# Optimization experiments

Measured on AMD Instinct MI355X. Metric: run time of the kernel, lower is better.

## Reference

```python
import jax, jax.numpy as jnp
import numpy as np

K = 16  # nsample for knn_point

def _bn(x, g, b):
    # inference-mode BatchNorm1d folded to per-channel affine (running stats 0/1)
    return x * g[None, :, None] + b[None, :, None]

def _knn(xyz, k):
    # xyz: [B,3,N] -> idx [B,N,k] of k nearest neighbors (squared L2)
    p = xyz.transpose(0, 2, 1)                                   # [B,N,3]
    sq = jnp.sum(p * p, axis=-1)                                 # [B,N]
    d = sq[:, :, None] + sq[:, None, :] - 2.0 * jnp.einsum('bnc,bmc->bnm', p, p)
    _, idx = jax.lax.top_k(-d, k)
    return idx

def _gather(hT, idx):
    # hT: [B,N,C], idx: [B,N,K] -> [B,N,K,C]
    return jax.vmap(lambda a, i: a[i])(hT, idx)

def setup_inputs():
    key = jax.random.key(0)
    ks = jax.random.split(key, 12)
    B, N, C = 16, 2048, 128
    def w(k, shape, fan):
        return jax.random.normal(k, shape, jnp.float32) * (1.0 / np.sqrt(fan))
    o = jnp.ones; z = jnp.zeros
    return {
        'points': jax.random.normal(ks[0], (B, 6, N), jnp.float32),
        'label': jax.random.uniform(ks[1], (B, 1, 16), jnp.float32),
        'We1': w(ks[2], (C, 6), 6), 'ge1': o(C), 'be1': z(C),
        'We2': w(ks[3], (C, C), C), 'ge2': o(C), 'be2': z(C),
        'W1': w(ks[4], (3, C, C), C), 'g1': o((3, C)), 'b1': z((3, C)),
        'W2': w(ks[5], (3, C, C), C), 'g2': o((3, C)), 'b2': z((3, C)),
        'Wf': w(ks[6], (1024, 3 * C), 3 * C), 'gf': o(1024), 'bf': z(1024),
        'Wl': w(ks[7], (64, 16), 16), 'gl': o(64), 'bl': z(64),
        'Wc1': w(ks[8], (512, 3136), 3136), 'bc1': z(512), 'gc1': o(512), 'bb1': z(512),
        'Wc2': w(ks[9], (256, 512), 512), 'bc2': z(256), 'gc2': o(256), 'bb2': z(256),
        'Wc3': w(ks[10], (50, 256), 256), 'bc3': z(50),
    }

def reference(points, label, We1, ge1, be1, We2, ge2, be2, W1, g1, b1, W2, g2, b2,
              Wf, gf, bf, Wl, gl, bl, Wc1, bc1, gc1, bb1, Wc2, bc2, gc2, bb2, Wc3, bc3):
    B, _, N = points.shape
    x = points[:, :6, :]
    xyz = x[:, :3, :]
    idx = _knn(xyz, K)                                            # [B,N,16]
    # input embedding: two conv1x1 + BN + ReLU
    h = jax.nn.relu(_bn(jnp.einsum('oc,bcn->bon', We1, x), ge1, be1))
    h = jax.nn.relu(_bn(jnp.einsum('oc,bcn->bon', We2, h), ge2, be2))
    xs = []
    for i in range(3):  # PVDSA_Res blocks (simplified: conv-BN-ReLU, kNN max-agg, conv-BN + residual)
        t = jax.nn.relu(_bn(jnp.einsum('oc,bcn->bon', W1[i], h), g1[i], b1[i]))
        nbr = _gather(t.transpose(0, 2, 1), idx)                  # [B,N,K,C]
        m = nbr.max(axis=2).transpose(0, 2, 1)                    # [B,C,N]
        h = jax.nn.relu(_bn(jnp.einsum('oc,bcn->bon', W2[i], m), g2[i], b2[i]) + h)
        xs.append(h)
    xcat = jnp.concatenate(xs, axis=1)                            # [B,384,N]
    xf = jax.nn.leaky_relu(_bn(jnp.einsum('oc,bcn->bon', Wf, xcat), gf, bf), 0.2)  # [B,1024,N]
    x_max = xf.max(axis=-1)                                       # [B,1024]
    x_avg = xf.mean(axis=-1)                                      # [B,1024]
    cls = jnp.broadcast_to(label.transpose(0, 2, 1), (B, 16, N))
    lab = jax.nn.leaky_relu(_bn(jnp.einsum('oc,bcn->bon', Wl, cls), gl, bl), 0.2)  # [B,64,N]
    glob = jnp.concatenate([
        jnp.broadcast_to(x_max[:, :, None], (B, 1024, N)),
        jnp.broadcast_to(x_avg[:, :, None], (B, 1024, N)),
        lab], axis=1)
    xa = jnp.concatenate([xf, glob], axis=1)                      # [B,3136,N]
    c = jax.nn.relu(_bn(jnp.einsum('oc,bcn->bon', Wc1, xa) + bc1[None, :, None], gc1, bb1))
    c = jax.nn.relu(_bn(jnp.einsum('oc,bcn->bon', Wc2, c) + bc2[None, :, None], gc2, bb2))
    out = jnp.einsum('oc,bcn->bon', Wc3, c) + bc3[None, :, None]  # [B,50,N]
    return out
```

## Files before the change

### kernel.cpp

```cpp
#include <hip/hip_runtime.h>
#include <cstdint>
#include <cstddef>

#define DEVINL __device__ __forceinline__

typedef float    f32x4 __attribute__((ext_vector_type(4)));
typedef _Float16 f16x8 __attribute__((ext_vector_type(8)));
typedef _Float16 f16x4 __attribute__((ext_vector_type(4)));

constexpr int BB = 16, NN = 2048, MM = 32768;

constexpr size_t OFF_WE1 = 0;
constexpr size_t OFF_WE2 = OFF_WE1 + 128 * 64 * 2;
constexpr size_t OFF_W1  = OFF_WE2 + 128 * 128 * 2;
constexpr size_t OFF_W2  = OFF_W1  + 3 * 128 * 128 * 2;
constexpr size_t OFF_WF  = OFF_W2  + 3 * 128 * 128 * 2;
constexpr size_t OFF_WC1 = OFF_WF  + 1024 * 384 * 2;
constexpr size_t OFF_WC2 = OFF_WC1 + 512 * 1024 * 2;
constexpr size_t OFF_WC3 = OFF_WC2 + 256 * 512 * 2;
constexpr size_t OFF_BC2 = OFF_WC3 + 128 * 256 * 2;
constexpr size_t OFF_BC3 = OFF_BC2 + 256 * 4;
constexpr size_t OFF_CVEC= OFF_BC3 + 128 * 4;
constexpr size_t OFF_PMAX= OFF_CVEC+ 16 * 512 * 4;
constexpr size_t OFF_PSUM= OFF_PMAX+ 16 * 16 * 1024 * 4;
constexpr size_t OFF_IDX = OFF_PSUM+ 16 * 16 * 1024 * 4;
constexpr size_t OFF_R1  = 8ull << 20;
constexpr size_t OFF_X0  = OFF_R1;
constexpr size_t OFF_HT  = OFF_R1 + (4ull  << 20);
constexpr size_t OFF_TT  = OFF_R1 + (12ull << 20);
constexpr size_t OFF_MT  = OFF_R1 + (20ull << 20);
constexpr size_t OFF_C1  = OFF_R1;
constexpr size_t OFF_XCAT= OFF_R1 + (32ull << 20);
constexpr size_t OFF_C2  = OFF_XCAT;
constexpr size_t OFF_XF  = OFF_XCAT + (24ull << 20);

__global__ __launch_bounds__(256) void fold_all_kernel(
    const float* We1, const float* ge1, const float* We2, const float* ge2,
    const float* W1,  const float* g1,  const float* W2,  const float* g2,
    const float* Wf,  const float* gf,  const float* Wc1, const float* gc1,
    const float* Wc2, const float* gc2, const float* Wc3,
    const float* gc2b, const float* bc2, const float* bb2, const float* bc3,
    const float* pts, char* ws)
{
    const int bid = blockIdx.x;
    const int tid = threadIdx.x;

    if (bid == 4704) {
        ((float*)(ws + OFF_BC2))[tid] = gc2b[tid] * bc2[tid] + bb2[tid];
        return;
    }
    if (bid == 4705) {
        if (tid < 128) ((float*)(ws + OFF_BC3))[tid] = (tid < 50) ? bc3[tid] : 0.f;
        return;
    }
    if (bid >= 4706) {
        int m = (bid - 4706) * 256 + tid;
        int b = m >> 11, n = m & 2047;
        const float* ps = pts + (size_t)b * 6 * 2048 + n;
        _Float16 tmp[64];
#pragma unroll
        for (int c = 0; c < 64; ++c) tmp[c] = (_Float16)0.f;
#pragma unroll
        for (int c = 0; c < 6; ++c) tmp[c] = (_Float16)ps[(size_t)c << 11];
        _Float16* dst = (_Float16*)(ws + OFF_X0) + (size_t)m * 64;
#pragma unroll
        for (int v = 0; v < 8; ++v) *(f16x8*)(dst + v * 8) = *(const f16x8*)(tmp + v * 8);
        return;
    }

    int id, base;
    if      (bid < 32)   { id = 0;  base = 0;    }
    else if (bid < 96)   { id = 1;  base = 32;   }
    else if (bid < 160)  { id = 2;  base = 96;   }
    else if (bid < 224)  { id = 3;  base = 160;  }
    else if (bid < 288)  { id = 4;  base = 224;  }
    else if (bid < 352)  { id = 5;  base = 288;  }
    else if (bid < 416)  { id = 6;  base = 352;  }
    else if (bid < 480)  { id = 7;  base = 416;  }
    else if (bid < 2016) { id = 8;  base = 480;  }
    else if (bid < 4064) { id = 9;  base = 2016; }
    else if (bid < 4576) { id = 10; base = 4064; }
    else                 { id = 11; base = 4576; }

    const float* src = nullptr; const float* g = nullptr; _Float16* dst = nullptr;
    int O = 0, K = 0, lds = 0, Kp = 0;
    switch (id) {
        case 0:  src = We1; g = ge1; O = 128; K = 6;    lds = 6;    Kp = 64;   dst = (_Float16*)(ws + OFF_WE1); break;
        case 1:  src = We2; g = ge2; O = 128; K = 128;  lds = 128;  Kp = 128;  dst = (_Float16*)(ws + OFF_WE2); break;
        case 2: case 3: case 4: {
            int i = id - 2;
            src = W1 + (size_t)i * 16384; g = g1 + i * 128; O = 128; K = 128; lds = 128; Kp = 128;
            dst = (_Float16*)(ws + OFF_W1) + (size_t)i * 16384; break; }
        case 5: case 6: case 7: {
            int i = id - 5;
            src = W2 + (size_t)i * 16384; g = g2 + i * 128; O = 128; K = 128; lds = 128; Kp = 128;
            dst = (_Float16*)(ws + OFF_W2) + (size_t)i * 16384; break; }
        case 8:  src = Wf;  g = gf;  O = 1024; K = 384;  lds = 384;  Kp = 384;  dst = (_Float16*)(ws + OFF_WF);  break;
        case 9:  src = Wc1; g = gc1; O = 512;  K = 1024; lds = 3136; Kp = 1024; dst = (_Float16*)(ws + OFF_WC1); break;
        case 10: src = Wc2; g = gc2; O = 256;  K = 512;  lds = 512;  Kp = 512;  dst = (_Float16*)(ws + OFF_WC2); break;
        default: src = Wc3; g = nullptr; O = 50; K = 256; lds = 256; Kp = 256;  dst = (_Float16*)(ws + OFF_WC3); break;
    }
    int e = (bid - base) * 256 + tid;
    int o = e / Kp, k = e - o * Kp;
    float v = 0.f;
    if (o < O && k < K) {
        v = src[(size_t)o * lds + k];
        if (g) v *= g[o];
    }
    dst[e] = (_Float16)v;
}

DEVINL float knn_dist(const float4 pq, const float4 pm) {
    float t = pq.x * pm.x;
    t = fmaf(pq.y, pm.y, t);
    t = fmaf(pq.z, pm.z, t);
    return fmaf(-2.f, t, pm.w);
}

#define KNN_DINS(X) do { \
    const float x_ = (X); \
    d15 = __builtin_amdgcn_fmed3f(x_, d14, d15); \
    d14 = __builtin_amdgcn_fmed3f(x_, d13, d14); \
    d13 = __builtin_amdgcn_fmed3f(x_, d12, d13); \
    d12 = __builtin_amdgcn_fmed3f(x_, d11, d12); \
    d11 = __builtin_amdgcn_fmed3f(x_, d10, d11); \
    d10 = __builtin_amdgcn_fmed3f(x_, d9,  d10); \
    d9  = __builtin_amdgcn_fmed3f(x_, d8,  d9);  \
    d8  = __builtin_amdgcn_fmed3f(x_, d7,  d8);  \
    d7  = __builtin_amdgcn_fmed3f(x_, d6,  d7);  \
    d6  = __builtin_amdgcn_fmed3f(x_, d5,  d6);  \
    d5  = __builtin_amdgcn_fmed3f(x_, d4,  d5);  \
    d4  = __builtin_amdgcn_fmed3f(x_, d3,  d4);  \
    d3  = __builtin_amdgcn_fmed3f(x_, d2,  d3);  \
    d2  = __builtin_amdgcn_fmed3f(x_, d1,  d2);  \
    d1  = __builtin_amdgcn_fmed3f(x_, d0,  d1);  \
    d0  = __builtin_amdgcn_fmed3f(x_, -3.4e38f, d0); \
} while (0)

#define KNN_CE(A, B) { const float lo_ = fminf(A, B), hi_ = fmaxf(A, B); A = lo_; B = hi_; }

#define KNN_MERGE(OFF) do { \
    const float n0  = __shfl_xor(d0,  OFF), n1  = __shfl_xor(d1,  OFF), \
                n2  = __shfl_xor(d2,  OFF), n3  = __shfl_xor(d3,  OFF), \
                n4  = __shfl_xor(d4,  OFF), n5  = __shfl_xor(d5,  OFF), \
                n6  = __shfl_xor(d6,  OFF), n7  = __shfl_xor(d7,  OFF), \
                n8  = __shfl_xor(d8,  OFF), n9  = __shfl_xor(d9,  OFF), \
                n10 = __shfl_xor(d10, OFF), n11 = __shfl_xor(d11, OFF), \
                n12 = __shfl_xor(d12, OFF), n13 = __shfl_xor(d13, OFF), \
                n14 = __shfl_xor(d14, OFF), n15 = __shfl_xor(d15, OFF); \
    d0  = fminf(d0,  n15); d1  = fminf(d1,  n14); d2  = fminf(d2,  n13); d3  = fminf(d3,  n12); \
    d4  = fminf(d4,  n11); d5  = fminf(d5,  n10); d6  = fminf(d6,  n9);  d7  = fminf(d7,  n8);  \
    d8  = fminf(d8,  n7);  d9  = fminf(d9,  n6);  d10 = fminf(d10, n5);  d11 = fminf(d11, n4);  \
    d12 = fminf(d12, n3);  d13 = fminf(d13, n2);  d14 = fminf(d14, n1);  d15 = fminf(d15, n0);  \
    KNN_CE(d0, d8)  KNN_CE(d1, d9)  KNN_CE(d2, d10) KNN_CE(d3, d11) \
    KNN_CE(d4, d12) KNN_CE(d5, d13) KNN_CE(d6, d14) KNN_CE(d7, d15) \
    KNN_CE(d0, d4)  KNN_CE(d1, d5)  KNN_CE(d2, d6)  KNN_CE(d3, d7)  \
    KNN_CE(d8, d12) KNN_CE(d9, d13) KNN_CE(d10,d14) KNN_CE(d11,d15) \
    KNN_CE(d0, d2)  KNN_CE(d1, d3)  KNN_CE(d4, d6)  KNN_CE(d5, d7)  \
    KNN_CE(d8, d10) KNN_CE(d9, d11) KNN_CE(d12,d14) KNN_CE(d13,d15) \
    KNN_CE(d0, d1)  KNN_CE(d2, d3)  KNN_CE(d4, d5)  KNN_CE(d6, d7)  \
    KNN_CE(d8, d9)  KNN_CE(d10,d11) KNN_CE(d12,d13) KNN_CE(d14,d15) \
} while (0)

__global__ __launch_bounds__(256) void knn_kernel(const float* __restrict__ pts, int* __restrict__ idxout)
{
    __shared__ float4 P[2048];
    __shared__ unsigned short buf[32][96];
    __shared__ int cnt[32];
    __shared__ int wcnt[32];
    const int tid = threadIdx.x;
    const int b = blockIdx.x;
    const float* pb = pts + (size_t)b * 6 * 2048;
    for (int i = tid; i < 2048; i += 256) {
        float x = pb[i];
        float y = pb[2048 + i];
        float z = pb[4096 + i];
        P[i] = make_float4(x, y, z, x * x + y * y + z * z);
    }
    if (tid < 32) { cnt[tid] = 0; wcnt[tid] = 0; }
    __syncthreads();

    const int p = tid & 7;
    const int g = tid >> 3;
    const int q = blockIdx.y * 32 + g;
    const float4 pq = P[q];

    float d0 = 3.4e38f, d1 = 3.4e38f, d2 = 3.4e38f, d3 = 3.4e38f;
#pragma unroll 4
    for (int it = 0; it < 256; ++it) {
        const float4 pm = P[it * 8 + p];
        const float x = knn_dist(pq, pm);
        d3 = __builtin_amdgcn_fmed3f(x, d2, d3);
        d2 = __builtin_amdgcn_fmed3f(x, d1, d2);
        d1 = __builtin_amdgcn_fmed3f(x, d0, d1);
        d0 = fminf(x, d0);
    }
    float d4 = 3.4e38f, d5 = 3.4e38f, d6 = 3.4e38f, d7 = 3.4e38f,
          d8 = 3.4e38f, d9 = 3.4e38f, d10 = 3.4e38f, d11 = 3.4e38f,
          d12 = 3.4e38f, d13 = 3.4e38f, d14 = 3.4e38f, d15 = 3.4e38f;
    KNN_MERGE(1);
    KNN_MERGE(2);
    KNN_MERGE(4);
    const float tub = d15;

#pragma unroll 4
    for (int it = 0; it < 256; ++it) {
        const int m = it * 8 + p;
        const float d = knn_dist(pq, P[m]);
        if (d <= tub) {
            const int pos = atomicAdd(&cnt[g], 1);
            if (pos < 96) buf[g][pos] = (unsigned short)m;
        }
    }
    int C = cnt[g];
    if (C > 96) C = 96;

    d0 = 3.4e38f; d1 = 3.4e38f; d2 = 3.4e38f; d3 = 3.4e38f;
    d4 = 3.4e38f; d5 = 3.4e38f; d6 = 3.4e38f; d7 = 3.4e38f;
    d8 = 3.4e38f; d9 = 3.4e38f; d10 = 3.4e38f; d11 = 3.4e38f;
    d12 = 3.4e38f; d13 = 3.4e38f; d14 = 3.4e38f; d15 = 3.4e38f;
    for (int j = p; j < C; j += 8) {
        const int m = buf[g][j];
        const float x = knn_dist(pq, P[m]);
        KNN_DINS(x);
    }
    KNN_MERGE(1);
    KNN_MERGE(2);
    KNN_MERGE(4);
    const float t = d15;

    int* op = idxout + (((size_t)(b << 11) + q) << 4);
    for (int j = p; j < C; j += 8) {
        const int m = buf[g][j];
        const float d = knn_dist(pq, P[m]);
        if (d <= t) {
            const int pos = atomicAdd(&wcnt[g], 1);
            if (pos < 16) op[pos] = m;
        }
    }
}

__global__ __launch_bounds__(512, 2) void gemm256(
    const _Float16* __restrict__ W, const _Float16* __restrict__ X,
    _Float16* __restrict__ Y, const float* __restrict__ bias,
    int Kp, int ldX, int ldY, int Opad, int act, int biasPerBatch,
    float* __restrict__ pmax, float* __restrict__ psum)
{
    __shared__ _Float16 SH[65536];
    const int tid  = threadIdx.x;
    const int lane = tid & 63, wave = tid >> 6;
    const int r = lane & 15, quad = lane >> 4;
    const int wo = wave & 3, wm = wave >> 2;
    const int m_blk = blockIdx.x * 256, o_blk = blockIdx.y * 256;
    const int nt = Kp >> 6;

    f32x4 acc[4][8];
#pragma unroll
    for (int a = 0; a < 4; ++a)
#pragma unroll
        for (int c = 0; c < 8; ++c) acc[a][c] = (f32x4){0.f, 0.f, 0.f, 0.f};

    auto STAGE_HALF = [&](int mat, int tile, int h) {
        const int d = tile & 1;
        _Float16* base = SH + (size_t)(((d * 2 + mat) * 2 + h) << 13);
#pragma unroll
        for (int i = 0; i < 2; ++i) {
            const int g  = ((wave * 2 + i) << 6) + lane;
            const int R  = g >> 2, s2 = g & 3;
            const int K4 = s2 ^ ((R >> 1) & 3);
            const int gk = (tile << 6) + (h << 5) + (K4 << 3);
            const _Float16* src = (mat == 0)
                ? W + (size_t)(o_blk + R) * Kp + gk
                : X + (size_t)(m_blk + R) * ldX + gk;
            __builtin_amdgcn_global_load_lds(
                (const __attribute__((address_space(1))) unsigned int*)src,
                (__attribute__((address_space(3))) unsigned int*)(base + ((wave * 2 + i) << 9)),
                16, 0, 0);
        }
    };

    STAGE_HALF(0, 0, 0); STAGE_HALF(1, 0, 0);
    STAGE_HALF(0, 0, 1); STAGE_HALF(1, 0, 1);
    if (nt > 1) { STAGE_HALF(0, 1, 0); STAGE_HALF(1, 1, 0); }

    f16x8 af[4];
    for (int t = 0; t < nt; ++t) {
        const int d = t & 1;
#pragma unroll
        for (int ph = 0; ph < 4; ++ph) {
            const int ks = ph >> 1, mh = ph & 1;
            if (ph == 0) {
                if (t == nt - 1) asm volatile("s_waitcnt vmcnt(4)" ::: "memory");
                else             asm volatile("s_waitcnt vmcnt(8)" ::: "memory");
            } else if (ph == 2) {
                if (t == nt - 1) asm volatile("s_waitcnt vmcnt(0)" ::: "memory");
                else             asm volatile("s_waitcnt vmcnt(8)" ::: "memory");
            }
            __builtin_amdgcn_sched_barrier(0);
            __builtin_amdgcn_s_barrier();
            __builtin_amdgcn_sched_barrier(0);

            if (mh == 0) {
#pragma unroll
                for (int oi = 0; oi < 4; ++oi) {
                    const int R  = (wo << 6) + (oi << 4) + r;
                    const int s2 = quad ^ ((R >> 1) & 3);
                    af[oi] = *(const f16x8*)(SH + (size_t)(((d * 2 + 0) * 2 + ks) << 13)
                                                + (size_t)(((R << 2) + s2) << 3));
                }
            }
            f16x8 bf[4];
#pragma unroll
            for (int j = 0; j < 4; ++j) {
                const int mi = (mh << 2) + j;
                const int R  = (wm << 7) + (mi << 4) + r;
                const int s2 = quad ^ ((R >> 1) & 3);
                bf[j] = *(const f16x8*)(SH + (size_t)(((d * 2 + 1) * 2 + ks) << 13)
                                            + (size_t)(((R << 2) + s2) << 3));
            }

            if (ph == 0)      { if (t + 1 < nt) STAGE_HALF(0, t + 1, 1); }
            else if (ph == 1) { if (t + 1 < nt) STAGE_HALF(1, t + 1, 1); }
            else if (ph == 2) { if (t + 2 < nt) STAGE_HALF(0, t + 2, 0); }
            else              { if (t + 2 < nt) STAGE_HALF(1, t + 2, 0); }

            __builtin_amdgcn_s_setprio(1);
#pragma unroll
            for (int oi = 0; oi < 4; ++oi)
#pragma unroll
                for (int j = 0; j < 4; ++j)
                    acc[oi][(mh << 2) + j] =
                        __builtin_amdgcn_mfma_f32_16x16x32_f16(af[oi], bf[j], acc[oi][(mh << 2) + j], 0, 0, 0);
            __builtin_amdgcn_s_setprio(0);
            __builtin_amdgcn_sched_barrier(0);
        }
    }
    __syncthreads();

    const int bb = biasPerBatch ? (m_blk >> 11) * Opad : 0;
    _Float16* OT = SH;
#pragma unroll
    for (int oi = 0; oi < 4; ++oi) {
        const int ol = (wo << 6) + (oi << 4) + (quad << 2);
        const f32x4 bv = *(const f32x4*)(bias + bb + o_blk + ol);
#pragma unroll
        for (int mi = 0; mi < 8; ++mi) {
            const int row = (wm << 7) + (mi << 4) + r;
            f32x4 v = acc[oi][mi] + bv;
            f16x4 ov;
#pragma unroll
            for (int j = 0; j < 4; ++j) {
                float x = v[j];
                if (act == 1)      x = (x > 0.f) ? x : 0.0f;
                else if (act == 2) x = (x > 0.f) ? x : 0.2f * x;
                ov[j] = (_Float16)x;
            }
            const int s = (ol >> 2) ^ (row & 31);
            *(f16x4*)(OT + row * 256 + s * 4) = ov;
        }
    }
    __syncthreads();
#pragma unroll
    for (int p2 = 0; p2 < 16; ++p2) {
        const int g = (p2 << 9) + tid;
        const int row = g >> 5, c = g & 31;
        const int s0 = ((c << 1)) ^ (row & 31);
        const int s1 = ((c << 1) | 1) ^ (row & 31);
        f16x4 a  = *(const f16x4*)(OT + row * 256 + s0 * 4);
        f16x4 b2 = *(const f16x4*)(OT + row * 256 + s1 * 4);
        f16x8 o8;
        o8[0] = a[0]; o8[1] = a[1]; o8[2] = a[2]; o8[3] = a[3];
        o8[4] = b2[0]; o8[5] = b2[1]; o8[6] = b2[2]; o8[7] = b2[3];
        *(f16x8*)(Y + (size_t)(m_blk + row) * ldY + o_blk + (c << 3)) = o8;
    }

    if (pmax) {
        const int cg = tid & 63, h8 = tid >> 6;
        float mx0 = -3.4e38f, mx1 = -3.4e38f, mx2 = -3.4e38f, mx3 = -3.4e38f;
        float sm0 = 0.f, sm1 = 0.f, sm2 = 0.f, sm3 = 0.f;
#pragma unroll
        for (int rr = 0; rr < 32; ++rr) {
            const int row = (h8 << 5) + rr;
            const f16x4 v = *(const f16x4*)(OT + row * 256 + ((cg ^ (row & 31)) << 2));
            const float x0 = (float)v[0], x1 = (float)v[1], x2 = (float)v[2], x3 = (float)v[3];
            mx0 = fmaxf(mx0, x0); sm0 += x0;
            mx1 = fmaxf(mx1, x1); sm1 += x1;
            mx2 = fmaxf(mx2, x2); sm2 += x2;
            mx3 = fmaxf(mx3, x3); sm3 += x3;
        }
        __syncthreads();
        float* PR = (float*)SH;
        float* pw = PR + (size_t)(((h8 << 8) + (cg << 2)) << 1);
        pw[0] = mx0; pw[1] = sm0; pw[2] = mx1; pw[3] = sm1;
        pw[4] = mx2; pw[5] = sm2; pw[6] = mx3; pw[7] = sm3;
        __syncthreads();
        if (tid < 256) {
            float M = -3.4e38f, S = 0.f;
#pragma unroll
            for (int h2 = 0; h2 < 8; ++h2) {
                M = fmaxf(M, PR[(size_t)(((h2 << 8) + tid) << 1)]);
                S += PR[(size_t)(((h2 << 8) + tid) << 1) + 1];
            }
            const int b2 = m_blk >> 11, mt = (m_blk >> 8) & 7;
            pmax[((size_t)((b2 << 3) + mt) << 10) + o_blk + tid] = M;
            psum[((size_t)((b2 << 3) + mt) << 10) + o_blk + tid] = S;
        }
    }
}

template<int TM>
__global__ __launch_bounds__(256) void gemm_tile(
    const _Float16* __restrict__ W, const _Float16* __restrict__ X,
    _Float16* __restrict__ Y, float* __restrict__ Y32,
    const float* __restrict__ bias, const _Float16* __restrict__ Res,
    int Kp, int ldX, int xoff, int ldY, int yoff, int Opad,
    int act, int biasPerBatch, int ldR, int roff, int Olimit)
{
    constexpr int MI = TM / 32;
    constexpr int ASZ = 128 * 64;
    constexpr int BSZ = TM * 64;
    __shared__ _Float16 SH[2 * (ASZ + BSZ)];

    const int tid  = threadIdx.x;
    const int lane = tid & 63, wave = tid >> 6;
    const int r = lane & 15, quad = lane >> 4;
    const int m_blk = blockIdx.x * TM, o_blk = blockIdx.y * 128;
    const int oh = (wave >> 1) * 64, mh = (wave & 1) * (TM / 2);

    f32x4 acc[4][MI];
#pragma unroll
    for (int a = 0; a < 4; ++a)
#pragma unroll
        for (int c = 0; c < MI; ++c) acc[a][c] = (f32x4){0.f, 0.f, 0.f, 0.f};

    const int srow  = wave * 8 + (lane >> 3);
    const int sslot = lane & 7;

    auto STAGE = [&](int bufi, int k0) {
        _Float16* As = SH + bufi * (ASZ + BSZ);
        _Float16* Bs = As + ASZ;
#pragma unroll
        for (int t = 0; t < 4; ++t) {
            const int rowA = t * 32 + srow;
            const int gk = k0 + ((sslot ^ (rowA & 7)) << 3);
            const _Float16* gA = W + (size_t)(o_blk + rowA) * Kp + gk;
            __builtin_amdgcn_global_load_lds(
                (const __attribute__((address_space(1))) unsigned int*)gA,
                (__attribute__((address_space(3))) unsigned int*)(As + t * 2048 + wave * 512),
                16, 0, 0);
        }
#pragma unroll
        for (int t = 0; t < TM / 32; ++t) {
            const int rowB = t * 32 + srow;
            const int gk = k0 + ((sslot ^ (rowB & 7)) << 3);
            const _Float16* gB = X + (size_t)(m_blk + rowB) * ldX + xoff + gk;
            __builtin_amdgcn_global_load_lds(
                (const __attribute__((address_space(1))) unsigned int*)gB,
                (__attribute__((address_space(3))) unsigned int*)(Bs + t * 2048 + wave * 512),
                16, 0, 0);
        }
    };

    const int nt = Kp >> 6;
    STAGE(0, 0);
    int cur = 0;
    for (int t = 0; t < nt; ++t) {
        if (t + 1 < nt) {
            STAGE(cur ^ 1, (t + 1) << 6);
            if constexpr (TM == 128) asm volatile("s_waitcnt vmcnt(8)" ::: "memory");
            else                     asm volatile("s_waitcnt vmcnt(6)" ::: "memory");
        } else {
            asm volatile("s_waitcnt vmcnt(0)" ::: "memory");
        }
        __builtin_amdgcn_sched_barrier(0);
        __builtin_amdgcn_s_barrier();
        asm volatile("" ::: "memory");

        const _Float16* As = SH + cur * (ASZ + BSZ);
        const _Float16* Bs = As + ASZ;
        __builtin_amdgcn_s_setprio(1);
#pragma unroll
        for (int ks = 0; ks < 2; ++ks) {
            f16x8 af[4], bf[MI];
#pragma unroll
            for (int oi = 0; oi < 4; ++oi) {
                const int row = oh + oi * 16 + r;
                const int slot = (ks * 4 + quad) ^ (row & 7);
                af[oi] = *(const f16x8*)(As + row * 64 + slot * 8);
            }
#pragma unroll
            for (int mi = 0; mi < MI; ++mi) {
                const int row = mh + mi * 16 + r;
                const int slot = (ks * 4 + quad) ^ (row & 7);
                bf[mi] = *(const f16x8*)(Bs + row * 64 + slot * 8);
            }
#pragma unroll
            for (int oi = 0; oi < 4; ++oi)
#pragma unroll
                for (int mi = 0; mi < MI; ++mi)
                    acc[oi][mi] = __builtin_amdgcn_mfma_f32_16x16x32_f16(af[oi], bf[mi], acc[oi][mi], 0, 0, 0);
        }
        __builtin_amdgcn_s_setprio(0);
        asm volatile("" ::: "memory");
        __builtin_amdgcn_s_barrier();
        cur ^= 1;
    }

    const int bb = biasPerBatch ? (m_blk >> 11) * Opad : 0;
    __syncthreads();

    if (Y32) {
#pragma unroll
        for (int oi = 0; oi < 4; ++oi) {
            const int og = o_blk + oh + oi * 16 + quad * 4;
            const f32x4 bv = *(const f32x4*)(bias + bb + og);
#pragma unroll
            for (int mi = 0; mi < MI; ++mi) {
                const int m = m_blk + mh + mi * 16 + r;
                const int bidx = m >> 11, n = m & 2047;
                f32x4 v = acc[oi][mi] + bv;
#pragma unroll
                for (int j = 0; j < 4; ++j) {
                    float x = v[j];
                    if (act == 1)      x = (x > 0.f) ? x : 0.0f;
                    else if (act == 2) x = (x > 0.f) ? x : 0.2f * x;
                    const int o = og + j;
                    if (o < Olimit)
                        Y32[((size_t)(bidx * 50 + o) << 11) + n] = x;
                }
            }
        }
        return;
    }

    _Float16* OT = SH;
#pragma unroll
    for (int oi = 0; oi < 4; ++oi) {
        const int ol = oh + oi * 16 + quad * 4;
        const f32x4 bv = *(const f32x4*)(bias + bb + o_blk + ol);
#pragma unroll
        for (int mi = 0; mi < MI; ++mi) {
            const int row = mh + mi * 16 + r;
            f32x4 v = acc[oi][mi] + bv;
            if (Res) {
                f16x4 rr = *(const f16x4*)(Res + (size_t)(m_blk + row) * ldR + roff + o_blk + ol);
#pragma unroll
                for (int j = 0; j < 4; ++j) v[j] += (float)rr[j];
            }
            f16x4 ov;
#pragma unroll
            for (int j = 0; j < 4; ++j) {
                float x = v[j];
                if (act == 1)      x = (x > 0.f) ? x : 0.0f;
                else if (act == 2) x = (x > 0.f) ? x : 0.2f * x;
                ov[j] = (_Float16)x;
            }
            const int s = ((ol >> 2) ^ (row & 31)) << 2;
            *(f16x4*)(OT + row * 128 + s) = ov;
        }
    }
    __syncthreads();
#pragma unroll
    for (int it2 = 0; it2 < TM / 16; ++it2) {
        const int row = it2 * 16 + (tid >> 4);
        const int c = tid & 15;
        const int s0 = ((c * 2) ^ (row & 31)) << 2;
        const int s1 = ((c * 2 + 1) ^ (row & 31)) << 2;
        f16x4 a = *(const f16x4*)(OT + row * 128 + s0);
        f16x4 b2 = *(const f16x4*)(OT + row * 128 + s1);
        f16x8 o8;
        o8[0] = a[0]; o8[1] = a[1]; o8[2] = a[2]; o8[3] = a[3];
        o8[4] = b2[0]; o8[5] = b2[1]; o8[6] = b2[2]; o8[7] = b2[3];
        *(f16x8*)(Y + (size_t)(m_blk + row) * ldY + yoff + o_blk + c * 8) = o8;
    }
}

typedef short s16x8 __attribute__((ext_vector_type(8)));
__global__ __launch_bounds__(256) void gather_max_kernel(
    const short* __restrict__ T, const int* __restrict__ idx, short* __restrict__ Mo)
{
    const int tid = threadIdx.x;
    const int p = blockIdx.x * 16 + (tid >> 4);
    const int l = tid & 15;
    const int b = p >> 11;
    const int* ip = idx + (size_t)p * 16;
    size_t row = (size_t)((b << 11) + ip[0]);
    s16x8 cur = *(const s16x8*)(T + row * 128 + l * 8);
    unsigned short best[8];
#pragma unroll
    for (int e = 0; e < 8; ++e) best[e] = (unsigned short)cur[e];
#pragma unroll
    for (int j = 1; j < 16; ++j) {
        row = (size_t)((b << 11) + ip[j]);
        s16x8 v = *(const s16x8*)(T + row * 128 + l * 8);
#pragma unroll
        for (int e = 0; e < 8; ++e) {
            unsigned short u = (unsigned short)v[e];
            if (u > best[e]) best[e] = u;
        }
    }
    s16x8 ov;
#pragma unroll
    for (int e = 0; e < 8; ++e) ov[e] = (short)best[e];
    *(s16x8*)(Mo + (size_t)p * 128 + l * 8) = ov;
}

__global__ __launch_bounds__(256) void cvec_kernel(
    const float* __restrict__ label, const float* __restrict__ Wl, const float* __restrict__ gl, const float* __restrict__ bl,
    const float* __restrict__ Wc1, const float* __restrict__ bc1, const float* __restrict__ gc1, const float* __restrict__ bb1,
    const float* __restrict__ pmax, const float* __restrict__ psum, float* __restrict__ cvec)
{
    __shared__ float v[2112];
    __shared__ float red[256];
    const int b = blockIdx.x, og = blockIdx.y, tid = threadIdx.x;
    for (int i = tid; i < 1024; i += 256) {
        float mx = -3.4e38f, sm = 0.f;
#pragma unroll
        for (int c = 0; c < 8; ++c) {
            mx = fmaxf(mx, pmax[((size_t)(b * 8 + c) << 10) + i]);
            sm += psum[((size_t)(b * 8 + c) << 10) + i];
        }
        v[i] = mx;
        v[1024 + i] = sm * (1.f / 2048.f);
    }
    if (tid < 64) {
        float s = 0.f;
        for (int i = 0; i < 16; ++i) s += Wl[tid * 16 + i] * label[b * 16 + i];
        s = gl[tid] * s + bl[tid];
        v[2048 + tid] = (s > 0.f) ? s : 0.2f * s;
    }
    __syncthreads();
    const int o = og * 64 + (tid >> 2), part = tid & 3;
    const float* wrow = Wc1 + (size_t)o * 3136 + 1024 + part * 528;
    float s = 0.f;
    for (int j = 0; j < 528; ++j) s += wrow[j] * v[part * 528 + j];
    red[tid] = s;
    __syncthreads();
    if (part == 0) {
        float tot = red[tid] + red[tid + 1] + red[tid + 2] + red[tid + 3];
        cvec[((size_t)b << 9) + o] = gc1[o] * (tot + bc1[o]) + bb1[o];
    }
}

extern "C" void kernel_launch(void* const* d_in, const int* in_sizes, int n_in,
                              void* d_out, int out_size, void* d_ws, size_t ws_size,
                              hipStream_t stream)
{
    (void)in_sizes; (void)n_in; (void)out_size; (void)ws_size;
    const float* points = (const float*)d_in[0];
    const float* label  = (const float*)d_in[1];
    const float* We1 = (const float*)d_in[2];
    const float* ge1 = (const float*)d_in[3];
    const float* be1 = (const float*)d_in[4];
    const float* We2 = (const float*)d_in[5];
    const float* ge2 = (const float*)d_in[6];
    const float* be2 = (const float*)d_in[7];
    const float* W1  = (const float*)d_in[8];
    const float* g1  = (const float*)d_in[9];
    const float* b1  = (const float*)d_in[10];
    const float* W2  = (const float*)d_in[11];
    const float* g2  = (const float*)d_in[12];
    const float* b2  = (const float*)d_in[13];
    const float* Wf  = (const float*)d_in[14];
    const float* gf  = (const float*)d_in[15];
    const float* bfv = (const float*)d_in[16];
    const float* Wl  = (const float*)d_in[17];
    const float* gl  = (const float*)d_in[18];
    const float* bl  = (const float*)d_in[19];
    const float* Wc1 = (const float*)d_in[20];
    const float* bc1 = (const float*)d_in[21];
    const float* gc1 = (const float*)d_in[22];
    const float* bb1 = (const float*)d_in[23];
    const float* Wc2 = (const float*)d_in[24];
    const float* bc2 = (const float*)d_in[25];
    const float* gc2 = (const float*)d_in[26];
    const float* bb2 = (const float*)d_in[27];
    const float* Wc3 = (const float*)d_in[28];
    const float* bc3 = (const float*)d_in[29];

    char* ws = (char*)d_ws;
    _Float16* hT  = (_Float16*)(ws + OFF_HT);
    _Float16* tT  = (_Float16*)(ws + OFF_TT);
    _Float16* mT  = (_Float16*)(ws + OFF_MT);
    _Float16* xct = (_Float16*)(ws + OFF_XCAT);
    _Float16* xf  = (_Float16*)(ws + OFF_XF);
    _Float16* c1  = (_Float16*)(ws + OFF_C1);
    _Float16* c2  = (_Float16*)(ws + OFF_C2);
    int*      idx = (int*)     (ws + OFF_IDX);
    _Float16* x0  = (_Float16*)(ws + OFF_X0);

    _Float16* wE1 = (_Float16*)(ws + OFF_WE1);
    _Float16* wE2 = (_Float16*)(ws + OFF_WE2);
    _Float16* w1f = (_Float16*)(ws + OFF_W1);
    _Float16* w2f = (_Float16*)(ws + OFF_W2);
    _Float16* wF  = (_Float16*)(ws + OFF_WF);
    _Float16* wC1 = (_Float16*)(ws + OFF_WC1);
    _Float16* wC2 = (_Float16*)(ws + OFF_WC2);
    _Float16* wC3 = (_Float16*)(ws + OFF_WC3);
    float* bC2 = (float*)(ws + OFF_BC2);
    float* bC3 = (float*)(ws + OFF_BC3);
    float* cv  = (float*)(ws + OFF_CVEC);
    float* pmx = (float*)(ws + OFF_PMAX);
    float* psm = (float*)(ws + OFF_PSUM);

    fold_all_kernel<<<dim3(4834), 256, 0, stream>>>(We1, ge1, We2, ge2, W1, g1, W2, g2,
                                                    Wf, gf, Wc1, gc1, Wc2, gc2, Wc3,
                                                    gc2, bc2, bb2, bc3, points, ws);
    knn_kernel<<<dim3(BB, NN / 32), 256, 0, stream>>>(points, idx);

    gemm_tile<64><<<dim3(512, 1), 256, 0, stream>>>(wE1, x0, tT, nullptr, be1, nullptr, 64, 64, 0, 128, 0, 128, 1, 0, 0, 0, 128);
    gemm_tile<64><<<dim3(512, 1), 256, 0, stream>>>(wE2, tT, hT, nullptr, be2, nullptr, 128, 128, 0, 128, 0, 128, 1, 0, 0, 0, 128);

    for (int i = 0; i < 3; ++i) {
        const _Float16* hin = (i == 0) ? hT : xct;
        int ldH  = (i == 0) ? 128 : 384;
        int offH = (i == 0) ? 0 : (i - 1) * 128;
        gemm_tile<64><<<dim3(512, 1), 256, 0, stream>>>(w1f + (size_t)i * 16384, hin, tT, nullptr, b1 + i * 128, nullptr,
                                                        128, ldH, offH, 128, 0, 128, 1, 0, 0, 0, 128);
        gather_max_kernel<<<dim3(MM / 16), 256, 0, stream>>>((const short*)tT, idx, (short*)mT);
        gemm_tile<64><<<dim3(512, 1), 256, 0, stream>>>(w2f + (size_t)i * 16384, mT, xct, nullptr, b2 + i * 128, hin,
                                                        128, 128, 0, 384, i * 128, 128, 1, 0, ldH, offH, 128);
    }

    gemm256<<<dim3(128, 4), 512, 0, stream>>>(wF, xct, xf, bfv, 384, 384, 1024, 1024, 2, 0, pmx, psm);

    cvec_kernel<<<dim3(BB, 8), 256, 0, stream>>>(label, Wl, gl, bl, Wc1, bc1, gc1, bb1, pmx, psm, cv);

    gemm256<<<dim3(128, 2), 512, 0, stream>>>(wC1, xf, c1, cv, 1024, 1024, 512, 512, 1, 1, nullptr, nullptr);

    gemm_tile<128><<<dim3(256, 2), 256, 0, stream>>>(wC2, c1, c2, nullptr, bC2, nullptr, 512, 512, 0, 256, 0, 256, 1, 0, 0, 0, 256);
    gemm_tile<128><<<dim3(256, 1), 256, 0, stream>>>(wC3, c2, nullptr, (float*)d_out, bC3, nullptr, 256, 256, 0, 0, 0, 128, 0, 0, 0, 0, 50);
}
```

Before: 397.6 us.

## Simplify gemm256 to a whole-tile double-buffered pipeline with 8-slot XOR swizzle

Replaces the four-phase half-tile staging schedule, which had finer-grained waits and barriers per phase, with a plain double buffer that stages a full 64-wide K tile of W and X per iteration. The LDS layout changes to a row-major 64-element row with an 8-slot XOR swizzle. This removes phase bookkeeping and two of the barriers per phase, but adds a trailing barrier each iteration. Load latency is also hidden less finely, since the next tile's prefetch is issued at the start of each iteration instead of being spread across phases.

After: 392.9 us. No clear change (-1.2%).

```diff
diff --git a/kernel.cpp b/kernel.cpp
--- a/kernel.cpp
+++ b/kernel.cpp
@@ -246,6 +246,7 @@
     int Kp, int ldX, int ldY, int Opad, int act, int biasPerBatch,
     float* __restrict__ pmax, float* __restrict__ psum)
 {
+    constexpr int ASZ = 256 * 64;
     __shared__ _Float16 SH[65536];
     const int tid  = threadIdx.x;
     const int lane = tid & 63, wave = tid >> 6;
@@ -260,80 +261,75 @@
 #pragma unroll
         for (int c = 0; c < 8; ++c) acc[a][c] = (f32x4){0.f, 0.f, 0.f, 0.f};
 
-    auto STAGE_HALF = [&](int mat, int tile, int h) {
-        const int d = tile & 1;
-        _Float16* base = SH + (size_t)(((d * 2 + mat) * 2 + h) << 13);
-#pragma unroll
-        for (int i = 0; i < 2; ++i) {
-            const int g  = ((wave * 2 + i) << 6) + lane;
-            const int R  = g >> 2, s2 = g & 3;
-            const int K4 = s2 ^ ((R >> 1) & 3);
-            const int gk = (tile << 6) + (h << 5) + (K4 << 3);
-            const _Float16* src = (mat == 0)
-                ? W + (size_t)(o_blk + R) * Kp + gk
-                : X + (size_t)(m_blk + R) * ldX + gk;
+    const int srow  = wave * 8 + (lane >> 3);
+    const int sslot = lane & 7;
+
+    auto STAGE = [&](int bufi, int k0) {
+        _Float16* As = SH + bufi * (2 * ASZ);
+        _Float16* Bs = As + ASZ;
+#pragma unroll
+        for (int t = 0; t < 4; ++t) {
+            const int rowA = t * 64 + srow;
+            const int gk = k0 + ((sslot ^ (rowA & 7)) << 3);
+            const _Float16* gA = W + (size_t)(o_blk + rowA) * Kp + gk;
             __builtin_amdgcn_global_load_lds(
-                (const __attribute__((address_space(1))) unsigned int*)src,
-                (__attribute__((address_space(3))) unsigned int*)(base + ((wave * 2 + i) << 9)),
+                (const __attribute__((address_space(1))) unsigned int*)gA,
+                (__attribute__((address_space(3))) unsigned int*)(As + t * 4096 + wave * 512),
                 16, 0, 0);
         }
+#pragma unroll
+        for (int t = 0; t < 4; ++t) {
+            const int rowB = t * 64 + srow;
+            const int gk = k0 + ((sslot ^ (rowB & 7)) << 3);
+            const _Float16* gB = X + (size_t)(m_blk + rowB) * ldX + gk;
+            __builtin_amdgcn_global_load_lds(
+                (const __attribute__((address_space(1))) unsigned int*)gB,
+                (__attribute__((address_space(3))) unsigned int*)(Bs + t * 4096 + wave * 512),
+                16, 0, 0);
+        }
     };
 
-    STAGE_HALF(0, 0, 0); STAGE_HALF(1, 0, 0);
-    STAGE_HALF(0, 0, 1); STAGE_HALF(1, 0, 1);
-    if (nt > 1) { STAGE_HALF(0, 1, 0); STAGE_HALF(1, 1, 0); }
-
-    f16x8 af[4];
+    STAGE(0, 0);
+    int cur = 0;
     for (int t = 0; t < nt; ++t) {
-        const int d = t & 1;
-#pragma unroll
-        for (int ph = 0; ph < 4; ++ph) {
-            const int ks = ph >> 1, mh = ph & 1;
-            if (ph == 0) {
-                if (t == nt - 1) asm volatile("s_waitcnt vmcnt(4)" ::: "memory");
-                else             asm volatile("s_waitcnt vmcnt(8)" ::: "memory");
-            } else if (ph == 2) {
-                if (t == nt - 1) asm volatile("s_waitcnt vmcnt(0)" ::: "memory");
-                else             asm volatile("s_waitcnt vmcnt(8)" ::: "memory");
-            }
-            __builtin_amdgcn_sched_barrier(0);
-            __builtin_amdgcn_s_barrier();
-            __builtin_amdgcn_sched_barrier(0);
-
-            if (mh == 0) {
-#pragma unroll
-                for (int oi = 0; oi < 4; ++oi) {
-                    const int R  = (wo << 6) + (oi << 4) + r;
-                    const int s2 = quad ^ ((R >> 1) & 3);
-                    af[oi] = *(const f16x8*)(SH + (size_t)(((d * 2 + 0) * 2 + ks) << 13)
-                                                + (size_t)(((R << 2) + s2) << 3));
-                }
-            }
-            f16x8 bf[4];
-#pragma unroll
-            for (int j = 0; j < 4; ++j) {
-                const int mi = (mh << 2) + j;
-                const int R  = (wm << 7) + (mi << 4) + r;
-                const int s2 = quad ^ ((R >> 1) & 3);
-                bf[j] = *(const f16x8*)(SH + (size_t)(((d * 2 + 1) * 2 + ks) << 13)
-                                            + (size_t)(((R << 2) + s2) << 3));
-            }
-
-            if (ph == 0)      { if (t + 1 < nt) STAGE_HALF(0, t + 1, 1); }
-            else if (ph == 1) { if (t + 1 < nt) STAGE_HALF(1, t + 1, 1); }
-            else if (ph == 2) { if (t + 2 < nt) STAGE_HALF(0, t + 2, 0); }
-            else              { if (t + 2 < nt) STAGE_HALF(1, t + 2, 0); }
-
-            __builtin_amdgcn_s_setprio(1);
+        if (t + 1 < nt) {
+            STAGE(cur ^ 1, (t + 1) << 6);
+            asm volatile("s_waitcnt vmcnt(8)" ::: "memory");
+        } else {
+            asm volatile("s_waitcnt vmcnt(0)" ::: "memory");
+        }
+        __builtin_amdgcn_sched_barrier(0);
+        __builtin_amdgcn_s_barrier();
+        asm volatile("" ::: "memory");
+
+        const _Float16* As = SH + cur * (2 * ASZ);
+        const _Float16* Bs = As + ASZ;
+        __builtin_amdgcn_s_setprio(1);
+#pragma unroll
+        for (int ks = 0; ks < 2; ++ks) {
+            f16x8 af[4], bf[8];
+#pragma unroll
+            for (int oi = 0; oi < 4; ++oi) {
+                const int row = (wo << 6) + (oi << 4) + r;
+                const int slot = (ks * 4 + quad) ^ (row & 7);
+                af[oi] = *(const f16x8*)(As + row * 64 + slot * 8);
+            }
+#pragma unroll
+            for (int mi = 0; mi < 8; ++mi) {
+                const int row = (wm << 7) + (mi << 4) + r;
+                const int slot = (ks * 4 + quad) ^ (row & 7);
+                bf[mi] = *(const f16x8*)(Bs + row * 64 + slot * 8);
+            }
 #pragma unroll
             for (int oi = 0; oi < 4; ++oi)
 #pragma unroll
-                for (int j = 0; j < 4; ++j)
-                    acc[oi][(mh << 2) + j] =
-                        __builtin_amdgcn_mfma_f32_16x16x32_f16(af[oi], bf[j], acc[oi][(mh << 2) + j], 0, 0, 0);
-            __builtin_amdgcn_s_setprio(0);
-            __builtin_amdgcn_sched_barrier(0);
-        }
+                for (int mi = 0; mi < 8; ++mi)
+                    acc[oi][mi] = __builtin_amdgcn_mfma_f32_16x16x32_f16(af[oi], bf[mi], acc[oi][mi], 0, 0, 0);
+        }
+        __builtin_amdgcn_s_setprio(0);
+        asm volatile("" ::: "memory");
+        __builtin_amdgcn_s_barrier();
+        cur ^= 1;
     }
     __syncthreads();
 
```
